# Kernel optimization log

Hardware: AMD Instinct MI355X
Metric: run time of the kernel (lower is better)

Reference implementation:

```python
import jax, jax.numpy as jnp
import numpy as np

T, B, D = 1024, 8, 1024
H, DH, FF = 16, 64, 4096
BG = 0.1  # GRU gating bias constant
SCALE = 1.0 / DH ** 0.5


def layer_norm(x, g, b, eps=1e-5):
    mu = jnp.mean(x, axis=-1, keepdims=True)
    var = jnp.var(x, axis=-1, keepdims=True)
    return (x - mu) * jax.lax.rsqrt(var + eps) * g + b


def gru_gate(x, y, W, U, bz):
    # W, U: [3, D, D] stacking (r, z, g) projections; bz: Uz bias
    r = jax.nn.sigmoid(y @ W[0] + x @ U[0])
    z = jax.nn.sigmoid(y @ W[1] + x @ U[1] + bz - BG)
    h = jnp.tanh(y @ W[2] + r * (x @ U[2]))
    return (1.0 - z) * x + z * h


def setup_inputs() -> dict:
    key = jax.random.key(0)
    ks = jax.random.split(key, 16)
    s = 0.02
    inp = {
        "x": jax.random.normal(ks[0], (T, B, D), jnp.float32),
        "Wq": jax.random.normal(ks[1], (D, H * DH), jnp.float32) * s,
        "Wk": jax.random.normal(ks[2], (D, H * DH), jnp.float32) * s,
        "Wv": jax.random.normal(ks[3], (D, H * DH), jnp.float32) * s,
        "Wo": jax.random.normal(ks[4], (H * DH, D), jnp.float32) * s,
        "ln1_g": jnp.ones((D,), jnp.float32),
        "ln1_b": jnp.zeros((D,), jnp.float32),
        "W1": jax.random.normal(ks[5], (D, FF), jnp.float32) * s,
        "b1": jnp.zeros((FF,), jnp.float32),
        "W2": jax.random.normal(ks[6], (FF, D), jnp.float32) * s,
        "b2": jnp.zeros((D,), jnp.float32),
        "ln2_g": jnp.ones((D,), jnp.float32),
        "ln2_b": jnp.zeros((D,), jnp.float32),
        "gate1_W": jax.random.normal(ks[7], (3, D, D), jnp.float32) * s,
        "gate1_U": jax.random.normal(ks[8], (3, D, D), jnp.float32) * s,
        "gate1_bz": jnp.zeros((D,), jnp.float32),
        "gate2_W": jax.random.normal(ks[9], (3, D, D), jnp.float32) * s,
        "gate2_U": jax.random.normal(ks[10], (3, D, D), jnp.float32) * s,
        "gate2_bz": jnp.zeros((D,), jnp.float32),
        "attn_mask": jnp.triu(jnp.ones((T, T), bool), k=1),  # causal: mask j > i
    }
    return inp


def reference(x, Wq, Wk, Wv, Wo, ln1_g, ln1_b, W1, b1, W2, b2,
              ln2_g, ln2_b, gate1_W, gate1_U, gate1_bz,
              gate2_W, gate2_U, gate2_bz, attn_mask):
    # --- multihead attention (pre_lnorm=True) ---
    xn = layer_norm(x, ln1_g, ln1_b)                     # [T,B,D]
    q = (xn @ Wq).reshape(T, B, H, DH)
    k = (xn @ Wk).reshape(T, B, H, DH)
    v = (xn @ Wv).reshape(T, B, H, DH)
    scores = jnp.einsum('ibhd,jbhd->ijbh', q, k) * SCALE  # [T,T,B,H]
    scores = jnp.where(attn_mask[:, :, None, None], -jnp.inf, scores)
    probs = jax.nn.softmax(scores, axis=1)
    attn = jnp.einsum('ijbh,jbhd->ibhd', probs, v).reshape(T, B, H * DH)
    src2 = attn @ Wo                                      # [T,B,D]
    # --- GRU gate 1 ---
    src = gru_gate(x, src2, gate1_W, gate1_U, gate1_bz)
    # --- positionwise FFN (pre_lnorm=True) ---
    sn = layer_norm(src, ln2_g, ln2_b)
    ff = jax.nn.relu(sn @ W1 + b1) @ W2 + b2
    # --- GRU gate 2 ---
    return gru_gate(src, ff, gate2_W, gate2_U, gate2_bz)
```

## Files before the change

kernel.cpp:

```cpp
#include <hip/hip_runtime.h>
#include <hip/hip_bf16.h>

#define T_  1024
#define B_  8
#define D_  1024
#define H_  16
#define DH_ 64
#define FF_ 4096
#define MROWS (T_*B_)

typedef __attribute__((ext_vector_type(8))) short short8;
typedef __attribute__((ext_vector_type(4))) float f32x4;
typedef __attribute__((ext_vector_type(4))) unsigned short us4;
typedef __attribute__((ext_vector_type(4))) unsigned int  u32x4;

__device__ __forceinline__ unsigned short f2b(float f){
  unsigned int u = __builtin_bit_cast(unsigned int, f);
  u += 0x7FFFu + ((u >> 16) & 1u);
  return (unsigned short)(u >> 16);
}
__device__ __forceinline__ float b2f(unsigned short h){
  unsigned int u = ((unsigned int)h) << 16;
  return __builtin_bit_cast(float, u);
}

__device__ __forceinline__ void glds16(const unsigned short* g, unsigned short* l){
  __builtin_amdgcn_global_load_lds(
    (const __attribute__((address_space(1))) unsigned int*)g,
    (__attribute__((address_space(3))) unsigned int*)l, 16, 0, 0);
}

enum { FRELU=1 };

__global__ __launch_bounds__(512, 2) void gemm256(
    const unsigned short* __restrict__ A1, const unsigned short* __restrict__ A2,
    int K1, long lda,
    const unsigned short* __restrict__ Bt, long ldb,
    unsigned short* __restrict__ C, long ldc,
    const float* __restrict__ bias, int K, int flags)
{
  constexpr int BM = 256, BK = 32;
  extern __shared__ char L[];

  int t = threadIdx.x, w = t >> 6, l = t & 63;

  int nx = gridDim.x;
  int nwg = nx * gridDim.y;
  int lin = blockIdx.y*nx + blockIdx.x;
  if (!(nwg & 7)) lin = (lin & 7)*(nwg >> 3) + (lin >> 3);
  int bx = lin % nx, by = lin / nx;
  int m0 = by*BM, n0 = bx*BM;

  int srow[2], sce[2];
  #pragma unroll
  for (int q=0;q<2;q++){
    int p  = q*8192 + w*1024 + l*16;
    int sp = p ^ (((p>>7)&3)<<4);
    srow[q] = sp >> 6;
    sce[q]  = (sp & 63) >> 1;
  }

  auto stage = [&](int buf, int kt){
    int k0 = kt*BK;
    const unsigned short* ap; int ko;
    if (k0 < K1){ ap = A1; ko = k0; } else { ap = A2; ko = k0 - K1; }
    char* ab = L + buf*32768;
    char* bb = ab + 16384;
    #pragma unroll
    for (int q=0;q<2;q++)
      glds16(ap + (long)(m0 + srow[q])*lda + ko + sce[q],
             (unsigned short*)(ab + q*8192 + w*1024));
    #pragma unroll
    for (int q=0;q<2;q++)
      glds16(Bt + (long)(n0 + srow[q])*ldb + k0 + sce[q],
             (unsigned short*)(bb + q*8192 + w*1024));
  };

  f32x4 acc[8][4];
  #pragma unroll
  for (int m=0;m<8;m++)
    #pragma unroll
    for (int n=0;n<4;n++) acc[m][n] = (f32x4){0.f,0.f,0.f,0.f};

  int wr = w >> 2, wc = w & 3;
  int fr = l & 15, fq = l >> 4;
  int nk = K / BK;

  stage(0, 0);
  stage(1, 1);
  asm volatile("s_waitcnt vmcnt(4)" ::: "memory");
  __builtin_amdgcn_s_barrier();
  asm volatile("" ::: "memory");

  int cur = 0;
  for (int kt = 0; kt < nk; ++kt){
    int nxt = cur + 2; if (nxt >= 3) nxt -= 3;
    if (kt + 2 < nk) stage(nxt, kt + 2);

    const char* ab = L + cur*32768;
    const char* bb = ab + 16384;
    short8 af[8], bf[4];
    #pragma unroll
    for (int n=0;n<4;n++){
      int r = wc*64 + n*16 + fr;
      bf[n] = *(const short8*)(bb + ((r*64 + fq*16) ^ (((r>>1)&3)<<4)));
    }
    #pragma unroll
    for (int m=0;m<8;m++){
      int r = wr*128 + m*16 + fr;
      af[m] = *(const short8*)(ab + ((r*64 + fq*16) ^ (((r>>1)&3)<<4)));
    }
    __builtin_amdgcn_s_setprio(1);
    #pragma unroll
    for (int m=0;m<8;m++)
      #pragma unroll
      for (int n=0;n<4;n++)
        acc[m][n] = __builtin_amdgcn_mfma_f32_16x16x32_bf16(af[m], bf[n], acc[m][n], 0,0,0);
    __builtin_amdgcn_s_setprio(0);

    if (kt + 2 < nk) asm volatile("s_waitcnt vmcnt(4)" ::: "memory");
    else             asm volatile("s_waitcnt vmcnt(0)" ::: "memory");
    __builtin_amdgcn_s_barrier();
    asm volatile("" ::: "memory");
    cur += 1; if (cur >= 3) cur -= 3;
  }

  int r0 = m0 + wr*128 + (fq << 2);
  int c0 = n0 + wc*64 + fr;
  #pragma unroll
  for (int m=0;m<8;m++)
    #pragma unroll
    for (int n=0;n<4;n++){
      int col = c0 + n*16;
      float bv = bias ? bias[col] : 0.f;
      #pragma unroll
      for (int j=0;j<4;j++){
        float v = acc[m][n][j] + bv;
        if (flags & FRELU) v = v > 0.f ? v : 0.f;
        C[(long)(r0 + m*16 + j)*ldc + col] = f2b(v);
      }
    }
}

__global__ __launch_bounds__(256) void gemm_bf16(
    const unsigned short* __restrict__ A1, const unsigned short* __restrict__ A2,
    int K1, long lda,
    const unsigned short* __restrict__ Bt, long ldb,
    unsigned short* __restrict__ C, long ldc,
    const float* __restrict__ bias, int K, int flags)
{
  constexpr int BM = 128, BK = 32;
  __shared__ unsigned short As[2][BM*BK];
  __shared__ unsigned short Bs[2][BM*BK];

  int t = threadIdx.x, w = t >> 6, l = t & 63;

  int nx = gridDim.x;
  int nwg = nx * gridDim.y;
  int lin = blockIdx.y*nx + blockIdx.x;
  if (!(nwg & 7)) lin = (lin & 7)*(nwg >> 3) + (lin >> 3);
  int bx = lin % nx, by = lin / nx;
  int m0 = by*BM, n0 = bx*BM;

  int arow = t >> 2;
  int acol = ((t & 3) ^ ((arow >> 1) & 3)) * 8;
  const unsigned short* a1p = A1 + (long)(m0 + arow)*lda + acol;
  const unsigned short* a2p = A2 + (long)(m0 + arow)*lda + acol - K1;
  const unsigned short* bp  = Bt + (long)(n0 + arow)*ldb + acol;

  auto stage = [&](int buf, int k0){
    const unsigned short* ap = (k0 < K1) ? a1p : a2p;
    glds16(ap + k0,          &As[buf][      w*512]);
    glds16(ap + 64*lda + k0, &As[buf][2048 + w*512]);
    glds16(bp + k0,          &Bs[buf][      w*512]);
    glds16(bp + 64*ldb + k0, &Bs[buf][2048 + w*512]);
  };

  f32x4 acc[4][4];
  #pragma unroll
  for (int m=0;m<4;m++)
    #pragma unroll
    for (int n=0;n<4;n++) acc[m][n] = (f32x4){0.f,0.f,0.f,0.f};

  int wm = (w >> 1) * 64, wn = (w & 1) * 64;
  int fr = l & 15, fk = (l >> 4) * 8;
  int nk = K / BK;

  stage(0, 0);
  __syncthreads();

  for (int kt = 0; kt < nk; ++kt){
    int cur = kt & 1;
    if (kt + 1 < nk) stage(cur ^ 1, (kt+1)*BK);

    short8 af[4], bf[4];
    #pragma unroll
    for (int m=0;m<4;m++){
      int rr = wm + m*16 + fr;
      af[m] = *(const short8*)&As[cur][rr*BK + (fk ^ ((((rr)>>1)&3)<<3))];
    }
    #pragma unroll
    for (int n=0;n<4;n++){
      int rr = wn + n*16 + fr;
      bf[n] = *(const short8*)&Bs[cur][rr*BK + (fk ^ ((((rr)>>1)&3)<<3))];
    }
    #pragma unroll
    for (int m=0;m<4;m++)
      #pragma unroll
      for (int n=0;n<4;n++)
        acc[m][n] = __builtin_amdgcn_mfma_f32_16x16x32_bf16(af[m], bf[n], acc[m][n], 0, 0, 0);

    __syncthreads();
  }

  int r0 = m0 + wm + ((l >> 4) << 2);
  int c0 = n0 + wn + fr;
  #pragma unroll
  for (int m=0;m<4;m++)
    #pragma unroll
    for (int n=0;n<4;n++){
      int col = c0 + n*16;
      float bv = bias ? bias[col] : 0.f;
      #pragma unroll
      for (int j=0;j<4;j++){
        float v = acc[m][n][j] + bv;
        if (flags & FRELU) v = v > 0.f ? v : 0.f;
        C[(long)(r0 + m*16 + j)*ldc + col] = f2b(v);
      }
    }
}

__global__ __launch_bounds__(256) void flash_attn(
  const unsigned short* __restrict__ qkv, const unsigned short* __restrict__ vT,
  unsigned short* __restrict__ O)
{
  int p = blockIdx.x, z = blockIdx.y;
  int b = z >> 4, h = z & 15;
  const unsigned short* Vz = vT + (long)z*DH_*T_;

  __shared__ unsigned short Ks[64*64];
  __shared__ unsigned short Vs[64*64];
  __shared__ unsigned short Ps[4][32][72];

  int t = threadIdx.x, w = t >> 6, l = t & 63;
  int fr = l & 15, fg = l >> 4;
  int srow = t >> 2, sc = (t & 3) * 16;

  for (int rep = 0; rep < 2; ++rep){
    int qt = rep ? (7 - p) : p;
    int q0 = qt*128 + w*32;

    short8 qf[2][2];
    #pragma unroll
    for (int m=0;m<2;m++)
      #pragma unroll
      for (int ks=0;ks<2;ks++)
        qf[m][ks] = *(const short8*)(qkv + ((long)(q0 + m*16 + fr)*B_ + b)*3072 + h*DH_ + ks*32 + fg*8);

    f32x4 oacc[2][4];
    float mr[2][4], lr[2][4];
    #pragma unroll
    for (int m=0;m<2;m++){
      #pragma unroll
      for (int n=0;n<4;n++) oacc[m][n] = (f32x4){0.f,0.f,0.f,0.f};
      #pragma unroll
      for (int j=0;j<4;j++){ mr[m][j] = -1e30f; lr[m][j] = 0.f; }
    }

    int nkv = (qt + 1) * 2;
    for (int kt = 0; kt < nkv; ++kt){
      int kv0 = kt * 64;
      __syncthreads();
      {
        const unsigned short* kg = qkv + ((long)(kv0+srow)*B_ + b)*3072 + 1024 + h*DH_ + sc;
        const unsigned short* vg = Vz + (long)srow*T_ + kv0 + sc;
        int rb = srow*128, sw = (srow & 7) << 4;
        *(u32x4*)((char*)Ks + ((rb + sc*2     ) ^ sw)) = *(const u32x4*)(kg);
        *(u32x4*)((char*)Ks + ((rb + sc*2 + 16) ^ sw)) = *(const u32x4*)(kg + 8);
        *(u32x4*)((char*)Vs + ((rb + sc*2     ) ^ sw)) = *(const u32x4*)(vg);
        *(u32x4*)((char*)Vs + ((rb + sc*2 + 16) ^ sw)) = *(const u32x4*)(vg + 8);
      }
      __syncthreads();

      if (kv0 <= q0 + 31){
        f32x4 sacc[2][4];
        #pragma unroll
        for (int m=0;m<2;m++)
          #pragma unroll
          for (int n=0;n<4;n++) sacc[m][n] = (f32x4){0.f,0.f,0.f,0.f};
        __builtin_amdgcn_s_setprio(1);
        #pragma unroll
        for (int ks=0;ks<2;ks++){
          short8 kf[4];
          #pragma unroll
          for (int n=0;n<4;n++){
            int r = n*16 + fr;
            kf[n] = *(const short8*)((const char*)Ks + ((r*128 + ks*64 + fg*16) ^ ((r & 7) << 4)));
          }
          #pragma unroll
          for (int m=0;m<2;m++)
            #pragma unroll
            for (int n=0;n<4;n++)
              sacc[m][n] = __builtin_amdgcn_mfma_f32_16x16x32_bf16(qf[m][ks], kf[n], sacc[m][n], 0,0,0);
        }
        __builtin_amdgcn_s_setprio(0);

        #pragma unroll
        for (int m=0;m<2;m++)
          #pragma unroll
          for (int j=0;j<4;j++){
            int qg = q0 + m*16 + fg*4 + j;
            float vmax = -1e30f;
            #pragma unroll
            for (int n=0;n<4;n++){
              int kg = kv0 + n*16 + fr;
              float s = (kg <= qg) ? sacc[m][n][j]*0.125f : -1e30f;
              sacc[m][n][j] = s;
              vmax = fmaxf(vmax, s);
            }
            #pragma unroll
            for (int msk=1; msk<16; msk<<=1) vmax = fmaxf(vmax, __shfl_xor(vmax, msk));
            float mnew = fmaxf(mr[m][j], vmax);
            float sc_o = __expf(mr[m][j] - mnew);
            mr[m][j] = mnew;
            float rsum = 0.f;
            #pragma unroll
            for (int n=0;n<4;n++){
              float pv = __expf(sacc[m][n][j] - mnew);
              sacc[m][n][j] = pv;
              rsum += pv;
            }
            #pragma unroll
            for (int msk=1; msk<16; msk<<=1) rsum += __shfl_xor(rsum, msk);
            lr[m][j] = lr[m][j]*sc_o + rsum;
            #pragma unroll
            for (int n=0;n<4;n++) oacc[m][n][j] *= sc_o;
          }

        #pragma unroll
        for (int m=0;m<2;m++)
          #pragma unroll
          for (int n=0;n<4;n++)
            #pragma unroll
            for (int j=0;j<4;j++)
              Ps[w][m*16 + fg*4 + j][n*16 + fr] = f2b(sacc[m][n][j]);

        __builtin_amdgcn_s_setprio(1);
        #pragma unroll
        for (int ks=0;ks<2;ks++){
          short8 pf[2], vf[4];
          #pragma unroll
          for (int m=0;m<2;m++) pf[m] = *(const short8*)&Ps[w][m*16+fr][ks*32+fg*8];
          #pragma unroll
          for (int n=0;n<4;n++){
            int r = n*16 + fr;
            vf[n] = *(const short8*)((const char*)Vs + ((r*128 + ks*64 + fg*16) ^ ((r & 7) << 4)));
          }
          #pragma unroll
          for (int m=0;m<2;m++)
            #pragma unroll
            for (int n=0;n<4;n++)
              oacc[m][n] = __builtin_amdgcn_mfma_f32_16x16x32_bf16(pf[m], vf[n], oacc[m][n], 0,0,0);
        }
        __builtin_amdgcn_s_setprio(0);
      }
    }

    #pragma unroll
    for (int m=0;m<2;m++)
      #pragma unroll
      for (int j=0;j<4;j++){
        float inv = 1.f / lr[m][j];
        long i = q0 + m*16 + fg*4 + j;
        #pragma unroll
        for (int n=0;n<4;n++)
          O[(i*B_ + b)*(long)D_ + h*DH_ + n*16 + fr] = f2b(oacc[m][n][j] * inv);
      }
  }
}

__global__ __launch_bounds__(256) void ln_cast(const float* __restrict__ X,
    const float* __restrict__ g, const float* __restrict__ bta,
    unsigned short* __restrict__ xn, unsigned short* __restrict__ xbf)
{
  long row = blockIdx.x;
  int t = threadIdx.x;
  f32x4 xv = ((const f32x4*)(X + row*D_))[t];
  float s = xv[0]+xv[1]+xv[2]+xv[3];
  float q = xv[0]*xv[0]+xv[1]*xv[1]+xv[2]*xv[2]+xv[3]*xv[3];
  #pragma unroll
  for (int o=32;o;o>>=1){ s += __shfl_xor(s,o); q += __shfl_xor(q,o); }
  __shared__ float rs[4], rq[4];
  int w = t >> 6;
  if ((t & 63) == 0){ rs[w]=s; rq[w]=q; }
  __syncthreads();
  s = rs[0]+rs[1]+rs[2]+rs[3];
  q = rq[0]+rq[1]+rq[2]+rq[3];
  float mean = s * (1.f/D_);
  float var  = q * (1.f/D_) - mean*mean;
  float rstd = rsqrtf(var + 1e-5f);
  f32x4 gv = ((const f32x4*)g)[t];
  f32x4 bv = ((const f32x4*)bta)[t];
  us4 o, raw;
  #pragma unroll
  for (int jj=0;jj<4;jj++){
    o[jj]   = f2b((xv[jj]-mean)*rstd*gv[jj] + bv[jj]);
    raw[jj] = f2b(xv[jj]);
  }
  ((us4*)(xn  + row*D_))[t] = o;
  ((us4*)(xbf + row*D_))[t] = raw;
}

__global__ __launch_bounds__(256) void tr_f2b(const float* __restrict__ src,
    unsigned short* __restrict__ dst, int N, long ldd)
{
  __shared__ float tile[32][33];
  int k0 = blockIdx.x*32, n0 = blockIdx.y*32;
  int tx = threadIdx.x & 31, ty = threadIdx.x >> 5;
  #pragma unroll
  for (int i=0;i<4;i++)
    tile[ty+i*8][tx] = src[(long)(k0+ty+i*8)*N + n0 + tx];
  __syncthreads();
  #pragma unroll
  for (int i=0;i<4;i++)
    dst[(long)(n0+ty+i*8)*ldd + k0 + tx] = f2b(tile[tx][ty+i*8]);
}

__global__ __launch_bounds__(256) void tr_gate(const float* __restrict__ gW,
    const float* __restrict__ gU, unsigned short* __restrict__ Wb)
{
  __shared__ float tile[32][33];
  int z = blockIdx.z;
  int c = z >> 1;
  const float* src = ((z & 1) ? gU : gW) + (size_t)c*1048576;
  unsigned short* dst; long ldd;
  if (c < 2){ dst = Wb + (size_t)c*(1024*2048) + (z&1)*1024; ldd = 2048; }
  else      { dst = Wb + (size_t)(4 + (z&1))*1048576;        ldd = 1024; }
  int k0 = blockIdx.x*32, n0 = blockIdx.y*32;
  int tx = threadIdx.x & 31, ty = threadIdx.x >> 5;
  #pragma unroll
  for (int i=0;i<4;i++)
    tile[ty+i*8][tx] = src[(long)(k0+ty+i*8)*1024 + n0 + tx];
  __syncthreads();
  #pragma unroll
  for (int i=0;i<4;i++)
    dst[(long)(n0+ty+i*8)*ldd + k0 + tx] = f2b(tile[tx][ty+i*8]);
}

__global__ __launch_bounds__(256) void build_vT(const unsigned short* __restrict__ vsrc,
                                                unsigned short* __restrict__ vT)
{
  __shared__ unsigned short tile[32][33];
  int z = blockIdx.z, b = z >> 4, h = z & 15;
  int t0 = blockIdx.x*32, d0 = blockIdx.y*32;
  int tx = threadIdx.x & 31, ty = threadIdx.x >> 5;
  #pragma unroll
  for (int i=0;i<4;i++)
    tile[ty+i*8][tx] = vsrc[((long)(t0+ty+i*8)*B_ + b)*3072 + h*DH_ + d0 + tx];
  __syncthreads();
  #pragma unroll
  for (int i=0;i<4;i++)
    vT[(long)z*DH_*T_ + (long)(d0+ty+i*8)*T_ + t0 + tx] = tile[tx][ty+i*8];
}

__global__ __launch_bounds__(256) void gru_combine(
  const unsigned short* __restrict__ rz,
  const unsigned short* __restrict__ ya, const unsigned short* __restrict__ xb,
  const float* __restrict__ xin, const float* __restrict__ bz,
  float* __restrict__ of, unsigned short* __restrict__ ob,
  const float* __restrict__ lng, const float* __restrict__ lnb,
  unsigned short* __restrict__ sn)
{
  int t = threadIdx.x;
  long row = blockIdx.x;
  long i = row*1024 + t*4;
  int col = t*4;
  us4 r4 = *(const us4*)(rz + row*2048 + col);
  us4 z4 = *(const us4*)(rz + row*2048 + 1024 + col);
  us4 a4 = *(const us4*)(ya + i);
  us4 b4 = *(const us4*)(xb + i);
  f32x4 xv = *(const f32x4*)(xin + i);
  f32x4 bzv = *(const f32x4*)(bz + col);
  f32x4 o;
  #pragma unroll
  for (int jj=0;jj<4;jj++){
    float r = 1.f/(1.f + __expf(-b2f(r4[jj])));
    float z = 1.f/(1.f + __expf(-(b2f(z4[jj]) + bzv[jj] - 0.1f)));
    float h = tanhf(b2f(a4[jj]) + r*b2f(b4[jj]));
    o[jj] = (1.f - z)*xv[jj] + z*h;
  }
  *(f32x4*)(of+i) = o;
  if (ob){
    us4 q;
    #pragma unroll
    for (int jj=0;jj<4;jj++) q[jj] = f2b(o[jj]);
    *(us4*)(ob+i) = q;
  }
  if (sn){
    float s = o[0]+o[1]+o[2]+o[3];
    float q = o[0]*o[0]+o[1]*o[1]+o[2]*o[2]+o[3]*o[3];
    #pragma unroll
    for (int off=32;off;off>>=1){ s += __shfl_xor(s,off); q += __shfl_xor(q,off); }
    __shared__ float rs[4], rq[4];
    int w = t >> 6;
    if ((t & 63) == 0){ rs[w]=s; rq[w]=q; }
    __syncthreads();
    s = rs[0]+rs[1]+rs[2]+rs[3];
    q = rq[0]+rq[1]+rq[2]+rq[3];
    float mean = s * (1.f/D_);
    float var  = q * (1.f/D_) - mean*mean;
    float rstd = rsqrtf(var + 1e-5f);
    f32x4 gv = ((const f32x4*)lng)[t];
    f32x4 bv = ((const f32x4*)lnb)[t];
    us4 oq;
    #pragma unroll
    for (int jj=0;jj<4;jj++) oq[jj] = f2b((o[jj]-mean)*rstd*gv[jj] + bv[jj]);
    *(us4*)(sn+i) = oq;
  }
}

extern "C" void kernel_launch(void* const* d_in, const int* in_sizes, int n_in,
                              void* d_out, int out_size, void* d_ws, size_t ws_size,
                              hipStream_t stream)
{
  const float* x    = (const float*)d_in[0];
  const float* Wq   = (const float*)d_in[1];
  const float* Wk   = (const float*)d_in[2];
  const float* Wv   = (const float*)d_in[3];
  const float* Wo   = (const float*)d_in[4];
  const float* ln1g = (const float*)d_in[5];
  const float* ln1b = (const float*)d_in[6];
  const float* W1   = (const float*)d_in[7];
  const float* b1   = (const float*)d_in[8];
  const float* W2   = (const float*)d_in[9];
  const float* b2   = (const float*)d_in[10];
  const float* ln2g = (const float*)d_in[11];
  const float* ln2b = (const float*)d_in[12];
  const float* g1W  = (const float*)d_in[13];
  const float* g1U  = (const float*)d_in[14];
  const float* g1bz = (const float*)d_in[15];
  const float* g2W  = (const float*)d_in[16];
  const float* g2U  = (const float*)d_in[17];
  const float* g2bz = (const float*)d_in[18];
  float* out = (float*)d_out;

  const size_t MB = 1u << 20;
  if (ws_size < 144*MB) return;
  char* base = (char*)d_ws;

  (void)hipFuncSetAttribute((const void*)gemm256,
                            hipFuncAttributeMaxDynamicSharedMemorySize, 98304);

  unsigned short* W    = (unsigned short*)(base);
  unsigned short* x_bf = (unsigned short*)(base + 16*MB);
  unsigned short* sbf  = (unsigned short*)(base + 32*MB);
  unsigned short* src2 = (unsigned short*)(base + 48*MB);
  unsigned short* qkv  = (unsigned short*)(base + 64*MB);
  unsigned short* vT   = (unsigned short*)(base + 112*MB);
  unsigned short* attn = (unsigned short*)(base + 128*MB);
  unsigned short* xn   = attn;
  unsigned short* rz   = (unsigned short*)(base + 64*MB);
  unsigned short* yab  = (unsigned short*)(base + 96*MB);
  unsigned short* xbb  = (unsigned short*)(base + 112*MB);
  unsigned short* sn   = x_bf;
  unsigned short* ff1  = (unsigned short*)(base + 80*MB);
  unsigned short* ffb  = src2;

  const size_t E1M = 1048576;
  unsigned short* BtRZ = W;
  unsigned short* W2g  = W + 4*E1M;
  unsigned short* U2g  = W + 5*E1M;
  unsigned short* W1T  = W;
  unsigned short* W2T  = W + 4*E1M;
  unsigned short* Wqkv = W;
  unsigned short* WoT  = W + 3*E1M;

  dim3 blk(256);
  auto G = [&](const unsigned short* A1, const unsigned short* A2, int K1, long lda,
               const unsigned short* Bt, long ldb, unsigned short* C, long ldc,
               const float* bias, int M, int N, int K, int flags){
    gemm_bf16<<<dim3(N/128, M/128), blk, 0, stream>>>(A1,A2,K1,lda,Bt,ldb,C,ldc,bias,K,flags);
  };
  auto G2 = [&](const unsigned short* A1, const unsigned short* A2, int K1, long lda,
                const unsigned short* Bt, long ldb, unsigned short* C, long ldc,
                const float* bias, int M, int N, int K, int flags){
    gemm256<<<dim3(N/256, M/256), dim3(512), 98304, stream>>>(A1,A2,K1,lda,Bt,ldb,C,ldc,bias,K,flags);
  };

  tr_f2b<<<dim3(32,32), blk, 0, stream>>>(Wq, Wqkv,          D_, D_);
  tr_f2b<<<dim3(32,32), blk, 0, stream>>>(Wk, Wqkv + 1*E1M,  D_, D_);
  tr_f2b<<<dim3(32,32), blk, 0, stream>>>(Wv, Wqkv + 2*E1M,  D_, D_);
  tr_f2b<<<dim3(32,32), blk, 0, stream>>>(Wo, WoT,           D_, D_);
  ln_cast<<<dim3(MROWS), blk, 0, stream>>>(x, ln1g, ln1b, xn, x_bf);

  G2(xn, xn, D_, D_, Wqkv, D_, qkv, 3072, nullptr, MROWS, 3072, D_, 0);
  build_vT<<<dim3(32,2,128), blk, 0, stream>>>(qkv + 2048, vT);
  flash_attn<<<dim3(4, B_*H_), blk, 0, stream>>>(qkv, vT, attn);
  G(attn, attn, D_, D_, WoT, D_, src2, D_, nullptr, MROWS, D_, D_, 0);

  tr_gate<<<dim3(32,32,6), blk, 0, stream>>>(g1W, g1U, W);
  G2(src2, x_bf, D_, D_, BtRZ, 2048, rz, 2048, nullptr, MROWS, 2048, 2048, 0);
  G(src2, src2, D_, D_, W2g, D_, yab, D_, nullptr, MROWS, D_, D_, 0);
  G(x_bf, x_bf, D_, D_, U2g, D_, xbb, D_, nullptr, MROWS, D_, D_, 0);
  gru_combine<<<dim3(MROWS), blk, 0, stream>>>(rz, yab, xbb, x, g1bz, out, sbf, ln2g, ln2b, sn);

  tr_f2b<<<dim3(32,128), blk, 0, stream>>>(W1, W1T, FF_, D_);
  tr_f2b<<<dim3(128,32), blk, 0, stream>>>(W2, W2T, D_, FF_);
  G2(sn, sn, D_, D_, W1T, D_, ff1, FF_, b1, MROWS, FF_, D_, FRELU);
  G(ff1, ff1, FF_, FF_, W2T, FF_, ffb, D_, b2, MROWS, D_, FF_, 0);

  tr_gate<<<dim3(32,32,6), blk, 0, stream>>>(g2W, g2U, W);
  G2(ffb, sbf, D_, D_, BtRZ, 2048, rz, 2048, nullptr, MROWS, 2048, 2048, 0);
  G(ffb, ffb, D_, D_, W2g, D_, yab, D_, nullptr, MROWS, D_, D_, 0);
  G(sbf, sbf, D_, D_, U2g, D_, xbb, D_, nullptr, MROWS, D_, D_, 0);
  gru_combine<<<dim3(MROWS), blk, 0, stream>>>(rz, yab, xbb, out, g2bz, out, nullptr, nullptr, nullptr, nullptr);
}
```

Measured before the change: 749.1 us.

## Deepen GEMM prefetch pipelines and merge gate y/x GEMMs into one launch

The 256-tile GEMM moves from a 3-stage to a 4-stage LDS ring buffer (128KB dynamic shared memory), and the 128-tile GEMM from double to triple buffering. Both use explicit vmcnt waits and skip the barrier on the final iteration. The two separate D×D gate GEMMs (y@W_g and x@U_g) now run as one 256-tile launch that picks the A and B operands per column block and writes into a shared [M,2048] buffer read by gru_combine. The goal is to hide more memory latency and cut launch count, at the cost of higher LDS use, which may lower occupancy for gemm256.

```diff
diff --git a/kernel.cpp b/kernel.cpp
--- a/kernel.cpp
+++ b/kernel.cpp
@@ -37,7 +37,9 @@
     int K1, long lda,
     const unsigned short* __restrict__ Bt, long ldb,
     unsigned short* __restrict__ C, long ldc,
-    const float* __restrict__ bias, int K, int flags)
+    const float* __restrict__ bias, int K, int flags,
+    const unsigned short* __restrict__ A1b, const unsigned short* __restrict__ Btb,
+    int N1)
 {
   constexpr int BM = 256, BK = 32;
   extern __shared__ char L[];
@@ -51,6 +53,11 @@
   int bx = lin % nx, by = lin / nx;
   int m0 = by*BM, n0 = bx*BM;
 
+  const unsigned short* Aa = A1;
+  const unsigned short* Ab = A2;
+  const unsigned short* Bb = Bt;
+  if (n0 >= N1){ Aa = A1b; Ab = A1b; Bb = Btb - (long)N1*ldb; }
+
   int srow[2], sce[2];
   #pragma unroll
   for (int q=0;q<2;q++){
@@ -63,7 +70,7 @@
   auto stage = [&](int buf, int kt){
     int k0 = kt*BK;
     const unsigned short* ap; int ko;
-    if (k0 < K1){ ap = A1; ko = k0; } else { ap = A2; ko = k0 - K1; }
+    if (k0 < K1){ ap = Aa; ko = k0; } else { ap = Ab; ko = k0 - K1; }
     char* ab = L + buf*32768;
     char* bb = ab + 16384;
     #pragma unroll
@@ -72,7 +79,7 @@
              (unsigned short*)(ab + q*8192 + w*1024));
     #pragma unroll
     for (int q=0;q<2;q++)
-      glds16(Bt + (long)(n0 + srow[q])*ldb + k0 + sce[q],
+      glds16(Bb + (long)(n0 + srow[q])*ldb + k0 + sce[q],
              (unsigned short*)(bb + q*8192 + w*1024));
   };
 
@@ -88,14 +95,14 @@
 
   stage(0, 0);
   stage(1, 1);
-  asm volatile("s_waitcnt vmcnt(4)" ::: "memory");
+  stage(2, 2);
+  asm volatile("s_waitcnt vmcnt(8)" ::: "memory");
   __builtin_amdgcn_s_barrier();
   asm volatile("" ::: "memory");
 
   int cur = 0;
   for (int kt = 0; kt < nk; ++kt){
-    int nxt = cur + 2; if (nxt >= 3) nxt -= 3;
-    if (kt + 2 < nk) stage(nxt, kt + 2);
+    if (kt + 3 < nk) stage((cur + 3) & 3, kt + 3);
 
     const char* ab = L + cur*32768;
     const char* bb = ab + 16384;
@@ -118,11 +125,15 @@
         acc[m][n] = __builtin_amdgcn_mfma_f32_16x16x32_bf16(af[m], bf[n], acc[m][n], 0,0,0);
     __builtin_amdgcn_s_setprio(0);
 
-    if (kt + 2 < nk) asm volatile("s_waitcnt vmcnt(4)" ::: "memory");
-    else             asm volatile("s_waitcnt vmcnt(0)" ::: "memory");
-    __builtin_amdgcn_s_barrier();
-    asm volatile("" ::: "memory");
-    cur += 1; if (cur >= 3) cur -= 3;
+    int c = nk - 1 - kt; if (c > 3) c = 3;
+    if (c == 3)      asm volatile("s_waitcnt vmcnt(8)" ::: "memory");
+    else if (c == 2) asm volatile("s_waitcnt vmcnt(4)" ::: "memory");
+    else if (c == 1) asm volatile("s_waitcnt vmcnt(0)" ::: "memory");
+    if (c > 0){
+      __builtin_amdgcn_s_barrier();
+      asm volatile("" ::: "memory");
+    }
+    cur = (cur + 1) & 3;
   }
 
   int r0 = m0 + wr*128 + (fq << 2);
@@ -150,8 +161,8 @@
     const float* __restrict__ bias, int K, int flags)
 {
   constexpr int BM = 128, BK = 32;
-  __shared__ unsigned short As[2][BM*BK];
-  __shared__ unsigned short Bs[2][BM*BK];
+  __shared__ unsigned short As[3][BM*BK];
+  __shared__ unsigned short Bs[3][BM*BK];
 
   int t = threadIdx.x, w = t >> 6, l = t & 63;
 
@@ -187,11 +198,15 @@
   int nk = K / BK;
 
   stage(0, 0);
-  __syncthreads();
-
+  stage(1, BK);
+  asm volatile("s_waitcnt vmcnt(4)" ::: "memory");
+  __builtin_amdgcn_s_barrier();
+  asm volatile("" ::: "memory");
+
+  int cur = 0;
   for (int kt = 0; kt < nk; ++kt){
-    int cur = kt & 1;
-    if (kt + 1 < nk) stage(cur ^ 1, (kt+1)*BK);
+    int nxt = cur + 2; if (nxt >= 3) nxt -= 3;
+    if (kt + 2 < nk) stage(nxt, (kt+2)*BK);
 
     short8 af[4], bf[4];
     #pragma unroll
@@ -210,7 +225,14 @@
       for (int n=0;n<4;n++)
         acc[m][n] = __builtin_amdgcn_mfma_f32_16x16x32_bf16(af[m], bf[n], acc[m][n], 0, 0, 0);
 
-    __syncthreads();
+    int c = nk - 1 - kt; if (c > 2) c = 2;
+    if (c == 2)      asm volatile("s_waitcnt vmcnt(4)" ::: "memory");
+    else if (c == 1) asm volatile("s_waitcnt vmcnt(0)" ::: "memory");
+    if (c > 0){
+      __builtin_amdgcn_s_barrier();
+      asm volatile("" ::: "memory");
+    }
+    cur += 1; if (cur >= 3) cur -= 3;
   }
 
   int r0 = m0 + wm + ((l >> 4) << 2);
@@ -465,7 +487,7 @@
 
 __global__ __launch_bounds__(256) void gru_combine(
   const unsigned short* __restrict__ rz,
-  const unsigned short* __restrict__ ya, const unsigned short* __restrict__ xb,
+  const unsigned short* __restrict__ yx,
   const float* __restrict__ xin, const float* __restrict__ bz,
   float* __restrict__ of, unsigned short* __restrict__ ob,
   const float* __restrict__ lng, const float* __restrict__ lnb,
@@ -477,8 +499,8 @@
   int col = t*4;
   us4 r4 = *(const us4*)(rz + row*2048 + col);
   us4 z4 = *(const us4*)(rz + row*2048 + 1024 + col);
-  us4 a4 = *(const us4*)(ya + i);
-  us4 b4 = *(const us4*)(xb + i);
+  us4 a4 = *(const us4*)(yx + row*2048 + col);
+  us4 b4 = *(const us4*)(yx + row*2048 + 1024 + col);
   f32x4 xv = *(const f32x4*)(xin + i);
   f32x4 bzv = *(const f32x4*)(bz + col);
   f32x4 o;
@@ -549,7 +571,7 @@
   char* base = (char*)d_ws;
 
   (void)hipFuncSetAttribute((const void*)gemm256,
-                            hipFuncAttributeMaxDynamicSharedMemorySize, 98304);
+                            hipFuncAttributeMaxDynamicSharedMemorySize, 131072);
 
   unsigned short* W    = (unsigned short*)(base);
   unsigned short* x_bf = (unsigned short*)(base + 16*MB);
@@ -560,8 +582,7 @@
   unsigned short* attn = (unsigned short*)(base + 128*MB);
   unsigned short* xn   = attn;
   unsigned short* rz   = (unsigned short*)(base + 64*MB);
-  unsigned short* yab  = (unsigned short*)(base + 96*MB);
-  unsigned short* xbb  = (unsigned short*)(base + 112*MB);
+  unsigned short* yx   = (unsigned short*)(base + 96*MB);
   unsigned short* sn   = x_bf;
   unsigned short* ff1  = (unsigned short*)(base + 80*MB);
   unsigned short* ffb  = src2;
@@ -575,6 +596,7 @@
   unsigned short* Wqkv = W;
   unsigned short* WoT  = W + 3*E1M;
 
+  const int NOSPLIT = 1 << 30;
   dim3 blk(256);
   auto G = [&](const unsigned short* A1, const unsigned short* A2, int K1, long lda,
                const unsigned short* Bt, long ldb, unsigned short* C, long ldc,
@@ -583,8 +605,10 @@
   };
   auto G2 = [&](const unsigned short* A1, const unsigned short* A2, int K1, long lda,
                 const unsigned short* Bt, long ldb, unsigned short* C, long ldc,
-                const float* bias, int M, int N, int K, int flags){
-    gemm256<<<dim3(N/256, M/256), dim3(512), 98304, stream>>>(A1,A2,K1,lda,Bt,ldb,C,ldc,bias,K,flags);
+                const float* bias, int M, int N, int K, int flags,
+                const unsigned short* A1b, const unsigned short* Btb, int N1){
+    gemm256<<<dim3(N/256, M/256), dim3(512), 131072, stream>>>(
+        A1,A2,K1,lda,Bt,ldb,C,ldc,bias,K,flags,A1b,Btb,N1);
   };
 
   tr_f2b<<<dim3(32,32), blk, 0, stream>>>(Wq, Wqkv,          D_, D_);
@@ -593,25 +617,23 @@
   tr_f2b<<<dim3(32,32), blk, 0, stream>>>(Wo, WoT,           D_, D_);
   ln_cast<<<dim3(MROWS), blk, 0, stream>>>(x, ln1g, ln1b, xn, x_bf);
 
-  G2(xn, xn, D_, D_, Wqkv, D_, qkv, 3072, nullptr, MROWS, 3072, D_, 0);
+  G2(xn, xn, D_, D_, Wqkv, D_, qkv, 3072, nullptr, MROWS, 3072, D_, 0, xn, Wqkv, NOSPLIT);
   build_vT<<<dim3(32,2,128), blk, 0, stream>>>(qkv + 2048, vT);
   flash_attn<<<dim3(4, B_*H_), blk, 0, stream>>>(qkv, vT, attn);
   G(attn, attn, D_, D_, WoT, D_, src2, D_, nullptr, MROWS, D_, D_, 0);
 
   tr_gate<<<dim3(32,32,6), blk, 0, stream>>>(g1W, g1U, W);
-  G2(src2, x_bf, D_, D_, BtRZ, 2048, rz, 2048, nullptr, MROWS, 2048, 2048, 0);
-  G(src2, src2, D_, D_, W2g, D_, yab, D_, nullptr, MROWS, D_, D_, 0);
-  G(x_bf, x_bf, D_, D_, U2g, D_, xbb, D_, nullptr, MROWS, D_, D_, 0);
-  gru_combine<<<dim3(MROWS), blk, 0, stream>>>(rz, yab, xbb, x, g1bz, out, sbf, ln2g, ln2b, sn);
+  G2(src2, x_bf, D_, D_, BtRZ, 2048, rz, 2048, nullptr, MROWS, 2048, 2048, 0, src2, BtRZ, NOSPLIT);
+  G2(src2, src2, D_, D_, W2g, D_, yx, 2048, nullptr, MROWS, 2048, D_, 0, x_bf, U2g, 1024);
+  gru_combine<<<dim3(MROWS), blk, 0, stream>>>(rz, yx, x, g1bz, out, sbf, ln2g, ln2b, sn);
 
   tr_f2b<<<dim3(32,128), blk, 0, stream>>>(W1, W1T, FF_, D_);
   tr_f2b<<<dim3(128,32), blk, 0, stream>>>(W2, W2T, D_, FF_);
-  G2(sn, sn, D_, D_, W1T, D_, ff1, FF_, b1, MROWS, FF_, D_, FRELU);
+  G2(sn, sn, D_, D_, W1T, D_, ff1, FF_, b1, MROWS, FF_, D_, FRELU, sn, W1T, NOSPLIT);
   G(ff1, ff1, FF_, FF_, W2T, FF_, ffb, D_, b2, MROWS, D_, FF_, 0);
 
   tr_gate<<<dim3(32,32,6), blk, 0, stream>>>(g2W, g2U, W);
-  G2(ffb, sbf, D_, D_, BtRZ, 2048, rz, 2048, nullptr, MROWS, 2048, 2048, 0);
-  G(ffb, ffb, D_, D_, W2g, D_, yab, D_, nullptr, MROWS, D_, D_, 0);
-  G(sbf, sbf, D_, D_, U2g, D_, xbb, D_, nullptr, MROWS, D_, D_, 0);
-  gru_combine<<<dim3(MROWS), blk, 0, stream>>>(rz, yab, xbb, out, g2bz, out, nullptr, nullptr, nullptr, nullptr);
-}
+  G2(ffb, sbf, D_, D_, BtRZ, 2048, rz, 2048, nullptr, MROWS, 2048, 2048, 0, ffb, BtRZ, NOSPLIT);
+  G2(ffb, ffb, D_, D_, W2g, D_, yx, 2048, nullptr, MROWS, 2048, D_, 0, sbf, U2g, 1024);
+  gru_combine<<<dim3(MROWS), blk, 0, stream>>>(rz, yx, out, g2bz, out, nullptr, nullptr, nullptr, nullptr);
+}
```

Result: faster. 716.6 us (-4.3%).
